# Kernel optimization log

Measured on AMD Instinct MI355X. Metric: run time of the kernel, lower is better.

Reference implementation:

```python
import jax, jax.numpy as jnp
import numpy as np

D_MODEL, D_BLOOM, N_HEADS = 768, 64, 4
HEAD_DIM = D_MODEL // N_HEADS


def setup_inputs() -> dict:
    key = jax.random.key(0)
    ks = jax.random.split(key, 16)
    B, S = 8, 1024
    s = 0.02
    return {
        "dnabert_hidden": jax.random.normal(ks[0], (B, S, D_MODEL), jnp.float32),
        "bloom_encoding": jax.random.uniform(ks[1], (B, S, D_BLOOM), jnp.float32),
        "Wq": jax.random.normal(ks[2], (D_MODEL, D_MODEL), jnp.float32) * s,
        "bq": jnp.zeros((D_MODEL,), jnp.float32),
        "Wk": jax.random.normal(ks[3], (D_BLOOM, D_MODEL), jnp.float32) * s,
        "bk": jnp.zeros((D_MODEL,), jnp.float32),
        "Wv": jax.random.normal(ks[4], (D_MODEL, D_MODEL), jnp.float32) * s,
        "bv": jnp.zeros((D_MODEL,), jnp.float32),
        "Wb1": jax.random.normal(ks[5], (D_BLOOM, N_HEADS * 2), jnp.float32) * s,
        "bb1": jnp.zeros((N_HEADS * 2,), jnp.float32),
        "Wb2": jax.random.normal(ks[6], (N_HEADS * 2, N_HEADS), jnp.float32) * s,
        "bb2": jnp.zeros((N_HEADS,), jnp.float32),
        "Wo": jax.random.normal(ks[7], (D_MODEL, D_MODEL), jnp.float32) * s,
        "bo": jnp.zeros((D_MODEL,), jnp.float32),
        "ln_g": jnp.ones((D_MODEL,), jnp.float32),
        "ln_b": jnp.zeros((D_MODEL,), jnp.float32),
    }


def reference(dnabert_hidden, bloom_encoding, Wq, bq, Wk, bk, Wv, bv,
              Wb1, bb1, Wb2, bb2, Wo, bo, ln_g, ln_b):
    B, S, _ = dnabert_hidden.shape
    H, Dh = N_HEADS, HEAD_DIM
    # projections -> [B, H, S, Dh]
    Q = (dnabert_hidden @ Wq + bq).reshape(B, S, H, Dh).transpose(0, 2, 1, 3)
    K = (bloom_encoding @ Wk + bk).reshape(B, S, H, Dh).transpose(0, 2, 1, 3)
    V = (dnabert_hidden @ Wv + bv).reshape(B, S, H, Dh).transpose(0, 2, 1, 3)
    scores = jnp.einsum('bhqd,bhkd->bhqk', Q, K) / jnp.sqrt(jnp.float32(Dh))
    # bloom bias MLP: [B, S, H] -> broadcast over query positions as [B, H, 1, S]
    h = jax.nn.gelu(bloom_encoding @ Wb1 + bb1, approximate=False)
    bias = (h @ Wb2 + bb2).transpose(0, 2, 1)[:, :, None, :]
    attn = jax.nn.softmax(scores + bias, axis=-1)  # dropout is identity in eval
    ctx = jnp.einsum('bhqk,bhkd->bhqd', attn, V)
    ctx = ctx.transpose(0, 2, 1, 3).reshape(B, S, H * Dh)
    out = ctx @ Wo + bo
    x = out + dnabert_hidden
    mu = jnp.mean(x, axis=-1, keepdims=True)
    var = jnp.var(x, axis=-1, keepdims=True)
    y = (x - mu) * jax.lax.rsqrt(var + 1e-5) * ln_g + ln_b
    return y, attn
```

## Files before the change

### kernel.cpp

```cpp
#include <hip/hip_runtime.h>
#include <hip/hip_bf16.h>
#include <math.h>
#include <stdint.h>

typedef __bf16 bf16;
typedef __bf16 bf16x8 __attribute__((ext_vector_type(8)));
typedef __bf16 bf16x4v __attribute__((ext_vector_type(4)));
typedef float f32x4 __attribute__((ext_vector_type(4)));

#define NHEADS 4
#define DM 768
#define DB 64
#define HD 192
#define BATCH 8
#define SEQ 1024
#define MROWS 8192
#define SCALE 0.07216878364870323f

__device__ __forceinline__ void gld_lds16(const void* g, void* l) {
  __builtin_amdgcn_global_load_lds(
      (__attribute__((address_space(1))) void*)(void*)g,
      (__attribute__((address_space(3))) void*)l, 16, 0, 0);
}

__global__ __launch_bounds__(256) void prologue(
    const float* __restrict__ Xd, bf16* __restrict__ Xd_bf,
    const float* __restrict__ Xb, bf16* __restrict__ Xb_bf,
    const float* __restrict__ Wq, const float* __restrict__ Wv,
    const float* __restrict__ Wk, const float* __restrict__ Wo,
    bf16* __restrict__ WT0, bf16* __restrict__ WT1,
    bf16* __restrict__ WT2, bf16* __restrict__ WT3,
    const float* __restrict__ Wb1, const float* __restrict__ bb1,
    const float* __restrict__ Wb2, const float* __restrict__ bb2,
    float* __restrict__ biasarr) {
  __shared__ float Lt[64 * 65];
  const int id = blockIdx.x;
  const int tid = threadIdx.x;
  if (id < 6656) {
    const float* in = (id < 6144) ? Xd : Xb;
    bf16* out = (id < 6144) ? Xd_bf : Xb_bf;
    long i = (long)(id < 6144 ? id : id - 6144) * 256 + tid;
    f32x4 v = *(const f32x4*)&in[i * 4];
    bf16x4v t;
    t[0] = (bf16)v[0]; t[1] = (bf16)v[1]; t[2] = (bf16)v[2]; t[3] = (bf16)v[3];
    *(bf16x4v*)&out[i * 4] = t;
  } else if (id < 6688) {
    int idx = (id - 6656) * 256 + tid;
    const float* x = Xb + (long)idx * DB;
    float h[8];
#pragma unroll
    for (int j = 0; j < 8; ++j) h[j] = bb1[j];
    for (int k = 0; k < DB; ++k) {
      float xv = x[k];
#pragma unroll
      for (int j = 0; j < 8; ++j) h[j] = fmaf(xv, Wb1[k * 8 + j], h[j]);
    }
#pragma unroll
    for (int j = 0; j < 8; ++j) {
      float a = h[j];
      h[j] = 0.5f * a * (1.0f + erff(a * 0.7071067811865476f));
    }
    int b = idx >> 10, s = idx & 1023;
#pragma unroll
    for (int o = 0; o < 4; ++o) {
      float a = bb2[o];
#pragma unroll
      for (int j = 0; j < 8; ++j) a = fmaf(h[j], Wb2[j * 4 + o], a);
      biasarr[((long)(b * 4 + o) << 10) + s] = a;
    }
  } else {
    int wi = id - 6688;
    const float* W;
    bf16* WT;
    int K, tIdx;
    if (wi < 144)      { W = Wq; WT = WT0; K = DM; tIdx = wi; }
    else if (wi < 288) { W = Wv; WT = WT1; K = DM; tIdx = wi - 144; }
    else if (wi < 300) { W = Wk; WT = WT2; K = DB; tIdx = wi - 288; }
    else               { W = Wo; WT = WT3; K = DM; tIdx = wi - 300; }
    const int tk0 = (tIdx / 12) * 64;
    const int tn0 = (tIdx % 12) * 64;
#pragma unroll
    for (int p = 0; p < 4; ++p) {
      int r = p * 16 + (tid >> 4);
      int c = (tid & 15) * 4;
      f32x4 v = *(const f32x4*)&W[(long)(tk0 + r) * DM + tn0 + c];
      Lt[r * 65 + c] = v[0]; Lt[r * 65 + c + 1] = v[1];
      Lt[r * 65 + c + 2] = v[2]; Lt[r * 65 + c + 3] = v[3];
    }
    __syncthreads();
    const int n = tid >> 2, kg = (tid & 3) * 16;
    bf16x8 o0, o1;
#pragma unroll
    for (int e = 0; e < 8; ++e) {
      o0[e] = (bf16)Lt[(kg + e) * 65 + n];
      o1[e] = (bf16)Lt[(kg + 8 + e) * 65 + n];
    }
    *(bf16x8*)&WT[(long)(tn0 + n) * K + tk0 + kg] = o0;
    *(bf16x8*)&WT[(long)(tn0 + n) * K + tk0 + kg + 8] = o1;
  }
}

__global__ __launch_bounds__(256) void rowsum_scale_f32(float* __restrict__ attn) {
  const int row = blockIdx.x * 4 + (threadIdx.x >> 6);
  const int lane = threadIdx.x & 63;
  float* ar = attn + ((long)row << 10);
  f32x4 v[4];
#pragma unroll
  for (int i = 0; i < 4; ++i) v[i] = *(const f32x4*)&ar[i * 256 + lane * 4];
  float s = 0.0f;
#pragma unroll
  for (int i = 0; i < 4; ++i)
#pragma unroll
    for (int j = 0; j < 4; ++j) s += v[i][j];
  for (int d = 1; d < 64; d <<= 1) s += __shfl_xor(s, d);
  float iv = 1.0f / s;
#pragma unroll
  for (int i = 0; i < 4; ++i) {
#pragma unroll
    for (int j = 0; j < 4; ++j) v[i][j] *= iv;
    *(f32x4*)&ar[i * 256 + lane * 4] = v[i];
  }
}

__global__ __launch_bounds__(256) void pv_attn(
    const bf16* __restrict__ E, const bf16* __restrict__ VT,
    const float* __restrict__ part, bf16* __restrict__ ctx,
    float* __restrict__ attn) {
  __shared__ __attribute__((aligned(16))) bf16 aL[2 * 64 * 32];
  __shared__ __attribute__((aligned(16))) bf16 bL[2 * 192 * 32];
  __shared__ float ivL[64];
  const int tid = threadIdx.x;
  const int lane = tid & 63;
  const int wid = tid >> 6;
  const int wr = wid >> 1, wc = wid & 1;
  const int id = blockIdx.x;
  const int bz = id & 31;
  const int by = id >> 5;
  const int m0 = by * 64;
  const int b = bz >> 2, h = bz & 3;

  const bf16* Ab = E + ((long)bz << 20);
  const bf16* Bb = VT + (((long)(b * DM + h * HD)) << 10);

  if (tid < 64) {
    const float* p = part + ((((long)bz << 10) + m0 + tid) << 4);
    float s = 0.0f;
#pragma unroll
    for (int i = 0; i < 16; ++i) s += p[i];
    ivL[tid] = 1.0f / s;
  }
  __syncthreads();
  const float iv0 = ivL[tid >> 2];

  f32x4 acc[2][6] = {};
  const int rsel = lane & 15, ksel = (lane >> 4) * 8;

  for (int k0 = 0; k0 < SEQ; k0 += 64) {
#pragma unroll
    for (int h2 = 0; h2 < 2; ++h2) {
      {
        int f = tid * 8;
        int row = f >> 5, col = f & 31;
        gld_lds16(Ab + (long)(m0 + row) * SEQ + k0 + h2 * 32 + col, &aL[h2 * 2048 + f]);
      }
#pragma unroll
      for (int p = 0; p < 3; ++p) {
        int f = (p * 256 + tid) * 8;
        int row = f >> 5, col = f & 31;
        gld_lds16(Bb + (long)row * SEQ + k0 + h2 * 32 + col, &bL[h2 * 6144 + f]);
      }
    }
    __syncthreads();

#pragma unroll
    for (int h2 = 0; h2 < 2; ++h2) {
      int f = tid * 8;
      int row = f >> 5, col = f & 31;
      bf16x8 e = *(const bf16x8*)&aL[h2 * 2048 + f];
      f32x4 w0, w1;
      w0[0] = (float)e[0] * iv0; w0[1] = (float)e[1] * iv0;
      w0[2] = (float)e[2] * iv0; w0[3] = (float)e[3] * iv0;
      w1[0] = (float)e[4] * iv0; w1[1] = (float)e[5] * iv0;
      w1[2] = (float)e[6] * iv0; w1[3] = (float)e[7] * iv0;
      float* ap = attn + ((long)bz << 20) + ((long)(m0 + row) << 10) + k0 + h2 * 32 + col;
      __builtin_nontemporal_store(w0, (f32x4*)ap);
      __builtin_nontemporal_store(w1, (f32x4*)(ap + 4));
    }

#pragma unroll
    for (int h2 = 0; h2 < 2; ++h2) {
      bf16x8 af[2], bfr[6];
#pragma unroll
      for (int m = 0; m < 2; ++m)
        af[m] = *(const bf16x8*)&aL[h2 * 2048 + (wr * 32 + m * 16 + rsel) * 32 + ksel];
#pragma unroll
      for (int n = 0; n < 6; ++n)
        bfr[n] = *(const bf16x8*)&bL[h2 * 6144 + (wc * 96 + n * 16 + rsel) * 32 + ksel];
#pragma unroll
      for (int m = 0; m < 2; ++m)
#pragma unroll
        for (int n = 0; n < 6; ++n)
          acc[m][n] = __builtin_amdgcn_mfma_f32_16x16x32_bf16(af[m], bfr[n], acc[m][n], 0, 0, 0);
    }
    __syncthreads();
  }

  const int rl = (lane >> 4) * 4, cl = lane & 15;
#pragma unroll
  for (int m = 0; m < 2; ++m)
#pragma unroll
    for (int n = 0; n < 6; ++n)
#pragma unroll
      for (int j = 0; j < 4; ++j) {
        int row = wr * 32 + m * 16 + rl + j;
        int col = wc * 96 + n * 16 + cl;
        bL[row * 192 + col] = (bf16)(acc[m][n][j] * ivL[row]);
      }
  __syncthreads();
#pragma unroll
  for (int it = 0; it < 6; ++it) {
    int idx2 = it * 256 + tid;
    int row = idx2 / 24;
    int col = (idx2 % 24) * 8;
    bf16x8 v = *(const bf16x8*)&bL[row * 192 + col];
    *(bf16x8*)&ctx[(long)(b * SEQ + m0 + row) * DM + h * HD + col] = v;
  }
}

template <int MODE>
__global__ __launch_bounds__(256) void gemm_bt(
    const bf16* __restrict__ A, int lda,
    const bf16* __restrict__ BT, int ldb,
    const float* __restrict__ Af,
    int M, int N, int Kd,
    const float* __restrict__ cb1,
    const float* __restrict__ cb2,
    const float* __restrict__ resid,
    void* __restrict__ out, void* __restrict__ out2) {
  __shared__ __attribute__((aligned(16))) bf16 aL[2 * 128 * 32];
  __shared__ __attribute__((aligned(16))) bf16 bL[2 * 128 * 32];
  const int tid = threadIdx.x;
  const int lane = tid & 63;
  const int wid = tid >> 6;
  const int wr = wid >> 1, wc = wid & 1;
  int bx, by, bz;
  if constexpr (MODE == 2 || MODE == 7) {
    int idd = blockIdx.x;
    bz = idd & 31;
    int t = idd >> 5;
    bx = t & 7;
    by = t >> 3;
  } else if constexpr (MODE == 5) {
    int idd = blockIdx.x;
    bz = idd & 31;
    bx = (idd >> 5) & 1;
    by = idd >> 6;
  } else {
    int idd = blockIdx.x;
    by = idd & 63;
    bx = idd >> 6;
    bz = 0;
  }
  const int m0 = by * 128, n0 = bx * 128;

  const bf16* Ab = A;
  const bf16* Bb = BT;
  const float* Afb = Af;
  if constexpr (MODE == 2 || MODE == 7) {
    long o = ((long)((bz >> 2) * SEQ)) * DM + (long)(bz & 3) * HD;
    Ab = A + o;
    Bb = BT + o;
  }
  if constexpr (MODE == 5) {
    Bb = BT + (((long)((bz >> 2) * DM + (bz & 3) * HD)) << 10);
    Afb = Af + ((long)bz << 20);
  }

  f32x4 acc[4][4] = {};

  for (int k0 = 0; k0 < Kd; k0 += 64) {
#pragma unroll
    for (int h = 0; h < 2; ++h) {
      if constexpr (MODE == 5) {
#pragma unroll
        for (int p = 0; p < 2; ++p) {
          int f = (p * 256 + tid) * 8;
          int row = f >> 5, col = f & 31;
          const float* g = Afb + (long)(m0 + row) * lda + k0 + h * 32 + col;
          f32x4 x0 = *(const f32x4*)g;
          f32x4 x1 = *(const f32x4*)(g + 4);
          bf16x8 t;
          t[0] = (bf16)x0[0]; t[1] = (bf16)x0[1]; t[2] = (bf16)x0[2]; t[3] = (bf16)x0[3];
          t[4] = (bf16)x1[0]; t[5] = (bf16)x1[1]; t[6] = (bf16)x1[2]; t[7] = (bf16)x1[3];
          *(bf16x8*)&aL[h * 4096 + f] = t;
        }
      } else {
#pragma unroll
        for (int p = 0; p < 2; ++p) {
          int f = (p * 256 + tid) * 8;
          int row = f >> 5, col = f & 31;
          gld_lds16(Ab + (long)(m0 + row) * lda + k0 + h * 32 + col, &aL[h * 4096 + f]);
        }
      }
#pragma unroll
      for (int p = 0; p < 2; ++p) {
        int f = (p * 256 + tid) * 8;
        int row = f >> 5, col = f & 31;
        int nn = n0 + row;
        nn = nn < N ? nn : N - 1;
        gld_lds16(Bb + (long)nn * ldb + k0 + h * 32 + col, &bL[h * 4096 + f]);
      }
    }
    __syncthreads();

    const int rsel = lane & 15, ksel = (lane >> 4) * 8;
#pragma unroll
    for (int h = 0; h < 2; ++h) {
      bf16x8 af[4], bfr[4];
#pragma unroll
      for (int m = 0; m < 4; ++m)
        af[m] = *(const bf16x8*)&aL[h * 4096 + (wr * 64 + m * 16 + rsel) * 32 + ksel];
#pragma unroll
      for (int n = 0; n < 4; ++n)
        bfr[n] = *(const bf16x8*)&bL[h * 4096 + (wc * 64 + n * 16 + rsel) * 32 + ksel];
#pragma unroll
      for (int m = 0; m < 4; ++m)
#pragma unroll
        for (int n = 0; n < 4; ++n)
          acc[m][n] = __builtin_amdgcn_mfma_f32_16x16x32_bf16(af[m], bfr[n], acc[m][n], 0, 0, 0);
    }
    __syncthreads();
  }

  const int rl = (lane >> 4) * 4, cl = lane & 15;

  if constexpr (MODE == 2) {
    float bvv[4];
#pragma unroll
    for (int n = 0; n < 4; ++n)
      bvv[n] = cb2[(bz << 10) + n0 + wc * 64 + n * 16 + cl];
#pragma unroll
    for (int m = 0; m < 4; ++m)
#pragma unroll
      for (int n = 0; n < 4; ++n)
#pragma unroll
        for (int j = 0; j < 4; ++j)
          acc[m][n][j] = __expf(fmaf(acc[m][n][j], SCALE, bvv[n]));
    float* part = (float*)out2;
#pragma unroll
    for (int m = 0; m < 4; ++m) {
#pragma unroll
      for (int j = 0; j < 4; ++j) {
        float s = acc[m][0][j] + acc[m][1][j] + acc[m][2][j] + acc[m][3][j];
#pragma unroll
        for (int d = 1; d < 16; d <<= 1) s += __shfl_xor(s, d);
        if (cl == 0) {
          int mg = m0 + wr * 64 + m * 16 + rl + j;
          part[((((long)bz << 10) + mg) << 4) + bx * 2 + wc] = s;
        }
      }
    }
#pragma unroll
    for (int m = 0; m < 4; ++m)
#pragma unroll
      for (int n = 0; n < 4; ++n)
#pragma unroll
        for (int j = 0; j < 4; ++j) {
          int row = wr * 64 + m * 16 + rl + j;
          int col = wc * 64 + n * 16 + cl;
          bf16* Lt = (row < 64) ? &aL[row * 128 + col] : &bL[(row - 64) * 128 + col];
          *Lt = (bf16)acc[m][n][j];
        }
    __syncthreads();
#pragma unroll
    for (int it = 0; it < 8; ++it) {
      int row = it * 16 + (tid >> 4);
      int col = (tid & 15) * 8;
      bf16x8 v = (row < 64) ? *(const bf16x8*)&aL[row * 128 + col]
                            : *(const bf16x8*)&bL[(row - 64) * 128 + col];
      *(bf16x8*)&((bf16*)out)[((long)bz << 20) + ((long)(m0 + row) << 10) + n0 + col] = v;
    }
    return;
  }

  if constexpr (MODE == 6) {
    if (n0 >= DM) {
      const int d0 = n0 - DM;
      float bvv[4];
#pragma unroll
      for (int n = 0; n < 4; ++n)
        bvv[n] = cb2[d0 + wc * 64 + n * 16 + cl];
#pragma unroll
      for (int m = 0; m < 4; ++m)
#pragma unroll
        for (int n = 0; n < 4; ++n)
#pragma unroll
          for (int j = 0; j < 4; ++j) {
            int row = wr * 64 + m * 16 + rl + j;
            int col = wc * 64 + n * 16 + cl;
            int sw = row ^ ((col & 7) << 4);
            bf16 val = (bf16)(acc[m][n][j] + bvv[n]);
            if (col < 64) aL[col * 128 + sw] = val;
            else          bL[(col - 64) * 128 + sw] = val;
          }
      __syncthreads();
      const int b = m0 >> 10, s0 = m0 & 1023;
#pragma unroll
      for (int it = 0; it < 8; ++it) {
        int d = it * 16 + (tid >> 4);
        int s = (tid & 15) * 8;
        int sw = s ^ ((d & 7) << 4);
        bf16x8 v = (d < 64) ? *(const bf16x8*)&aL[d * 128 + sw]
                            : *(const bf16x8*)&bL[(d - 64) * 128 + sw];
        *(bf16x8*)&((bf16*)out2)[((long)(b * DM + d0 + d) << 10) + s0 + s] = v;
      }
      return;
    }
  }

  if constexpr (MODE == 0 || MODE == 6) {
    float bvv[4];
#pragma unroll
    for (int n = 0; n < 4; ++n)
      bvv[n] = cb1[n0 + wc * 64 + n * 16 + cl];
#pragma unroll
    for (int m = 0; m < 4; ++m)
#pragma unroll
      for (int n = 0; n < 4; ++n)
#pragma unroll
        for (int j = 0; j < 4; ++j) {
          int row = wr * 64 + m * 16 + rl + j;
          int col = wc * 64 + n * 16 + cl;
          bf16 val = (bf16)(acc[m][n][j] + bvv[n]);
          if (row < 64) aL[row * 128 + col] = val;
          else          bL[(row - 64) * 128 + col] = val;
        }
    __syncthreads();
#pragma unroll
    for (int it = 0; it < 8; ++it) {
      int row = it * 16 + (tid >> 4);
      int col = (tid & 15) * 8;
      bf16x8 v = (row < 64) ? *(const bf16x8*)&aL[row * 128 + col]
                            : *(const bf16x8*)&bL[(row - 64) * 128 + col];
      *(bf16x8*)&((bf16*)out)[(long)(m0 + row) * DM + n0 + col] = v;
    }
    return;
  }

#pragma unroll
  for (int m = 0; m < 4; ++m) {
#pragma unroll
    for (int n = 0; n < 4; ++n) {
      int ng = n0 + wc * 64 + n * 16 + cl;
      if (ng >= N) continue;
#pragma unroll
      for (int j = 0; j < 4; ++j) {
        int mg = m0 + wr * 64 + m * 16 + rl + j;
        float v = acc[m][n][j];
        if constexpr (MODE == 7) {
          ((float*)out)[((long)bz << 20) + ((long)mg << 10) + ng] =
              __expf(fmaf(v, SCALE, cb2[(bz << 10) + ng]));
        } else if constexpr (MODE == 5) {
          ((bf16*)out)[(long)((bz >> 2) * SEQ + mg) * DM + (bz & 3) * HD + ng] = (bf16)v;
        } else {
          long o = (long)mg * DM + ng;
          ((float*)out)[o] = v + cb1[ng] + resid[o];
        }
      }
    }
  }
}

__global__ __launch_bounds__(256) void layernorm_rows(float* x, const float* __restrict__ gam,
                                                      const float* __restrict__ bet) {
  int row = blockIdx.x * 4 + (threadIdx.x >> 6);
  int lane = threadIdx.x & 63;
  float* r = x + (long)row * DM;
  f32x4 v[3];
#pragma unroll
  for (int i = 0; i < 3; ++i) v[i] = *(const f32x4*)&r[i * 256 + lane * 4];
  float s = 0.0f, ss = 0.0f;
#pragma unroll
  for (int i = 0; i < 3; ++i)
#pragma unroll
    for (int j = 0; j < 4; ++j) {
      s += v[i][j];
      ss += v[i][j] * v[i][j];
    }
  for (int d = 1; d < 64; d <<= 1) {
    s += __shfl_xor(s, d);
    ss += __shfl_xor(ss, d);
  }
  float mu = s * (1.0f / 768.0f);
  float var = ss * (1.0f / 768.0f) - mu * mu;
  float rs = 1.0f / sqrtf(var + 1e-5f);
#pragma unroll
  for (int i = 0; i < 3; ++i) {
#pragma unroll
    for (int j = 0; j < 4; ++j) {
      int c = i * 256 + lane * 4 + j;
      v[i][j] = (v[i][j] - mu) * rs * gam[c] + bet[c];
    }
    *(f32x4*)&r[i * 256 + lane * 4] = v[i];
  }
}

extern "C" void kernel_launch(void* const* d_in, const int* in_sizes, int n_in,
                              void* d_out, int out_size, void* d_ws, size_t ws_size,
                              hipStream_t stream) {
  const float* Xd = (const float*)d_in[0];
  const float* Xb = (const float*)d_in[1];
  const float* Wq = (const float*)d_in[2];
  const float* bq = (const float*)d_in[3];
  const float* Wk = (const float*)d_in[4];
  const float* bk = (const float*)d_in[5];
  const float* Wv = (const float*)d_in[6];
  const float* bv = (const float*)d_in[7];
  const float* Wb1 = (const float*)d_in[8];
  const float* bb1 = (const float*)d_in[9];
  const float* Wb2 = (const float*)d_in[10];
  const float* bb2 = (const float*)d_in[11];
  const float* Wo = (const float*)d_in[12];
  const float* bo = (const float*)d_in[13];
  const float* lng = (const float*)d_in[14];
  const float* lnb = (const float*)d_in[15];

  float* y = (float*)d_out;
  float* attn = y + (long)MROWS * DM;

  char* w = (char*)d_ws;
  bf16* Xd_bf = (bf16*)w; w += (long)MROWS * DM * 2;
  bf16* Xb_bf = (bf16*)w; w += (long)MROWS * DB * 2;
  bf16* WqvT = (bf16*)w; w += (long)2 * DM * DM * 2;
  bf16* WkT = (bf16*)w; w += (long)DM * DB * 2;
  bf16* WoT = (bf16*)w; w += (long)DM * DM * 2;
  bf16* Qb = (bf16*)w; w += (long)MROWS * DM * 2;
  bf16* Kb = (bf16*)w; w += (long)MROWS * DM * 2;
  bf16* VTb = (bf16*)w; w += (long)MROWS * DM * 2;
  float* biasarr = (float*)w; w += (long)BATCH * NHEADS * SEQ * 4;
  float* part = (float*)w; w += (long)32 * SEQ * 16 * 4;
  bf16* Sb = (bf16*)w; w += (long)32 * SEQ * SEQ * 2;
  const bool useS = ((size_t)(w - (char*)d_ws)) <= ws_size;
  bf16* ctxb = Xd_bf;

  dim3 blk(256);
  prologue<<<7132, blk, 0, stream>>>(Xd, Xd_bf, Xb, Xb_bf, Wq, Wv, Wk, Wo,
                                     WqvT, WqvT + (long)DM * DM, WkT, WoT,
                                     Wb1, bb1, Wb2, bb2, biasarr);

  gemm_bt<0><<<384, blk, 0, stream>>>(Xb_bf, DB, WkT, DB, nullptr, MROWS, DM, DB,
                                      bk, nullptr, nullptr, Kb, nullptr);
  gemm_bt<6><<<768, blk, 0, stream>>>(Xd_bf, DM, WqvT, DM, nullptr, MROWS, 2 * DM, DM,
                                      bq, bv, nullptr, Qb, VTb);
  if (useS) {
    gemm_bt<2><<<2048, blk, 0, stream>>>(Qb, DM, Kb, DM, nullptr, SEQ, SEQ, HD,
                                         nullptr, biasarr, nullptr, Sb, part);
    pv_attn<<<512, blk, 0, stream>>>(Sb, VTb, part, ctxb, attn);
  } else {
    gemm_bt<7><<<2048, blk, 0, stream>>>(Qb, DM, Kb, DM, nullptr, SEQ, SEQ, HD,
                                         nullptr, biasarr, nullptr, attn, nullptr);
    rowsum_scale_f32<<<8192, blk, 0, stream>>>(attn);
    gemm_bt<5><<<512, blk, 0, stream>>>(nullptr, SEQ, VTb, SEQ, attn, SEQ, HD, SEQ,
                                        nullptr, nullptr, nullptr, ctxb, nullptr);
  }
  gemm_bt<4><<<384, blk, 0, stream>>>(ctxb, DM, WoT, DM, nullptr, MROWS, DM, DM,
                                      bo, nullptr, Xd, y, nullptr);
  layernorm_rows<<<2048, 256, 0, stream>>>(y, lng, lnb);
}
```

Baseline: 175.7 us.

## Merge K and QV projection GEMMs into one launch; stage Wo epilogue via LDS

Replaces the two projection GEMM launches (K from the bloom encoding, Q/V from the hidden states) with a single kernel whose blocks branch by block index. This saves one launch and lets the small K blocks fill the tail of the larger Q/V work. The Wo GEMM epilogue now stages fp32 accumulators through shared memory in two halves, so the bias-plus-residual add and the output store become coalesced 16-byte accesses instead of scalar strided writes. The risks are extra barriers and shared-memory traffic in the epilogue. The merged kernel also uses a simple single-stage load loop that may differ from the original gemm_bt pipelining.

```diff
diff --git a/kernel.cpp b/kernel.cpp
--- a/kernel.cpp
+++ b/kernel.cpp
@@ -97,6 +97,137 @@
     }
     *(bf16x8*)&WT[(long)(tn0 + n) * K + tk0 + kg] = o0;
     *(bf16x8*)&WT[(long)(tn0 + n) * K + tk0 + kg + 8] = o1;
+  }
+}
+
+__global__ __launch_bounds__(256) void proj_all(
+    const bf16* __restrict__ Xb_bf, const bf16* __restrict__ WkT,
+    const bf16* __restrict__ Xd_bf, const bf16* __restrict__ WqvT,
+    const float* __restrict__ bk, const float* __restrict__ bq,
+    const float* __restrict__ bv,
+    bf16* __restrict__ Kb, bf16* __restrict__ Qb, bf16* __restrict__ VTb) {
+  __shared__ __attribute__((aligned(16))) bf16 aL[2 * 128 * 32];
+  __shared__ __attribute__((aligned(16))) bf16 bL[2 * 128 * 32];
+  const int tid = threadIdx.x;
+  const int lane = tid & 63;
+  const int wid = tid >> 6;
+  const int wr = wid >> 1, wc = wid & 1;
+  const int id = blockIdx.x;
+  const bool isK = id < 384;
+  int by, bx, lda, Kd, N;
+  const bf16 *A, *BT;
+  if (isK) {
+    by = id & 63; bx = id >> 6;
+    A = Xb_bf; BT = WkT; lda = DB; Kd = DB; N = DM;
+  } else {
+    int t = id - 384;
+    by = t & 63; bx = t >> 6;
+    A = Xd_bf; BT = WqvT; lda = DM; Kd = DM; N = 2 * DM;
+  }
+  const int m0 = by * 128, n0 = bx * 128;
+
+  f32x4 acc[4][4] = {};
+
+  for (int k0 = 0; k0 < Kd; k0 += 64) {
+#pragma unroll
+    for (int h = 0; h < 2; ++h) {
+#pragma unroll
+      for (int p = 0; p < 2; ++p) {
+        int f = (p * 256 + tid) * 8;
+        int row = f >> 5, col = f & 31;
+        gld_lds16(A + (long)(m0 + row) * lda + k0 + h * 32 + col, &aL[h * 4096 + f]);
+      }
+#pragma unroll
+      for (int p = 0; p < 2; ++p) {
+        int f = (p * 256 + tid) * 8;
+        int row = f >> 5, col = f & 31;
+        int nn = n0 + row;
+        nn = nn < N ? nn : N - 1;
+        gld_lds16(BT + (long)nn * lda + k0 + h * 32 + col, &bL[h * 4096 + f]);
+      }
+    }
+    __syncthreads();
+
+    const int rsel = lane & 15, ksel = (lane >> 4) * 8;
+#pragma unroll
+    for (int h = 0; h < 2; ++h) {
+      bf16x8 af[4], bfr[4];
+#pragma unroll
+      for (int m = 0; m < 4; ++m)
+        af[m] = *(const bf16x8*)&aL[h * 4096 + (wr * 64 + m * 16 + rsel) * 32 + ksel];
+#pragma unroll
+      for (int n = 0; n < 4; ++n)
+        bfr[n] = *(const bf16x8*)&bL[h * 4096 + (wc * 64 + n * 16 + rsel) * 32 + ksel];
+#pragma unroll
+      for (int m = 0; m < 4; ++m)
+#pragma unroll
+        for (int n = 0; n < 4; ++n)
+          acc[m][n] = __builtin_amdgcn_mfma_f32_16x16x32_bf16(af[m], bfr[n], acc[m][n], 0, 0, 0);
+    }
+    __syncthreads();
+  }
+
+  const int rl = (lane >> 4) * 4, cl = lane & 15;
+
+  if (!isK && n0 >= DM) {
+    const int d0 = n0 - DM;
+    float bvv[4];
+#pragma unroll
+    for (int n = 0; n < 4; ++n)
+      bvv[n] = bv[d0 + wc * 64 + n * 16 + cl];
+#pragma unroll
+    for (int m = 0; m < 4; ++m)
+#pragma unroll
+      for (int n = 0; n < 4; ++n)
+#pragma unroll
+        for (int j = 0; j < 4; ++j) {
+          int row = wr * 64 + m * 16 + rl + j;
+          int col = wc * 64 + n * 16 + cl;
+          int sw = row ^ ((col & 7) << 4);
+          bf16 val = (bf16)(acc[m][n][j] + bvv[n]);
+          if (col < 64) aL[col * 128 + sw] = val;
+          else          bL[(col - 64) * 128 + sw] = val;
+        }
+    __syncthreads();
+    const int b = m0 >> 10, s0 = m0 & 1023;
+#pragma unroll
+    for (int it = 0; it < 8; ++it) {
+      int d = it * 16 + (tid >> 4);
+      int s = (tid & 15) * 8;
+      int sw = s ^ ((d & 7) << 4);
+      bf16x8 v = (d < 64) ? *(const bf16x8*)&aL[d * 128 + sw]
+                          : *(const bf16x8*)&bL[(d - 64) * 128 + sw];
+      *(bf16x8*)&VTb[((long)(b * DM + d0 + d) << 10) + s0 + s] = v;
+    }
+    return;
+  }
+
+  const float* cb = isK ? bk : bq;
+  bf16* out = isK ? Kb : Qb;
+  float bvv[4];
+#pragma unroll
+  for (int n = 0; n < 4; ++n)
+    bvv[n] = cb[n0 + wc * 64 + n * 16 + cl];
+#pragma unroll
+  for (int m = 0; m < 4; ++m)
+#pragma unroll
+    for (int n = 0; n < 4; ++n)
+#pragma unroll
+      for (int j = 0; j < 4; ++j) {
+        int row = wr * 64 + m * 16 + rl + j;
+        int col = wc * 64 + n * 16 + cl;
+        bf16 val = (bf16)(acc[m][n][j] + bvv[n]);
+        if (row < 64) aL[row * 128 + col] = val;
+        else          bL[(row - 64) * 128 + col] = val;
+      }
+  __syncthreads();
+#pragma unroll
+  for (int it = 0; it < 8; ++it) {
+    int row = it * 16 + (tid >> 4);
+    int col = (tid & 15) * 8;
+    bf16x8 v = (row < 64) ? *(const bf16x8*)&aL[row * 128 + col]
+                          : *(const bf16x8*)&bL[(row - 64) * 128 + col];
+    *(bf16x8*)&out[(long)(m0 + row) * DM + n0 + col] = v;
   }
 }
 
@@ -383,66 +514,41 @@
     return;
   }
 
-  if constexpr (MODE == 6) {
-    if (n0 >= DM) {
-      const int d0 = n0 - DM;
-      float bvv[4];
-#pragma unroll
-      for (int n = 0; n < 4; ++n)
-        bvv[n] = cb2[d0 + wc * 64 + n * 16 + cl];
-#pragma unroll
-      for (int m = 0; m < 4; ++m)
-#pragma unroll
-        for (int n = 0; n < 4; ++n)
-#pragma unroll
-          for (int j = 0; j < 4; ++j) {
-            int row = wr * 64 + m * 16 + rl + j;
-            int col = wc * 64 + n * 16 + cl;
-            int sw = row ^ ((col & 7) << 4);
-            bf16 val = (bf16)(acc[m][n][j] + bvv[n]);
-            if (col < 64) aL[col * 128 + sw] = val;
-            else          bL[(col - 64) * 128 + sw] = val;
-          }
+  if constexpr (MODE == 4) {
+#pragma unroll
+    for (int half = 0; half < 2; ++half) {
+      if (wr == half) {
+#pragma unroll
+        for (int m = 0; m < 4; ++m)
+#pragma unroll
+          for (int n = 0; n < 4; ++n)
+#pragma unroll
+            for (int j = 0; j < 4; ++j) {
+              int r = m * 16 + rl + j;
+              int col = wc * 64 + n * 16 + cl;
+              float* Lf = (r < 32) ? (float*)aL + r * 128
+                                   : (float*)bL + (r - 32) * 128;
+              Lf[col] = acc[m][n][j];
+            }
+      }
       __syncthreads();
-      const int b = m0 >> 10, s0 = m0 & 1023;
 #pragma unroll
       for (int it = 0; it < 8; ++it) {
-        int d = it * 16 + (tid >> 4);
-        int s = (tid & 15) * 8;
-        int sw = s ^ ((d & 7) << 4);
-        bf16x8 v = (d < 64) ? *(const bf16x8*)&aL[d * 128 + sw]
-                            : *(const bf16x8*)&bL[(d - 64) * 128 + sw];
-        *(bf16x8*)&((bf16*)out2)[((long)(b * DM + d0 + d) << 10) + s0 + s] = v;
-      }
-      return;
-    }
-  }
-
-  if constexpr (MODE == 0 || MODE == 6) {
-    float bvv[4];
-#pragma unroll
-    for (int n = 0; n < 4; ++n)
-      bvv[n] = cb1[n0 + wc * 64 + n * 16 + cl];
-#pragma unroll
-    for (int m = 0; m < 4; ++m)
-#pragma unroll
-      for (int n = 0; n < 4; ++n)
-#pragma unroll
-        for (int j = 0; j < 4; ++j) {
-          int row = wr * 64 + m * 16 + rl + j;
-          int col = wc * 64 + n * 16 + cl;
-          bf16 val = (bf16)(acc[m][n][j] + bvv[n]);
-          if (row < 64) aL[row * 128 + col] = val;
-          else          bL[(row - 64) * 128 + col] = val;
-        }
-    __syncthreads();
-#pragma unroll
-    for (int it = 0; it < 8; ++it) {
-      int row = it * 16 + (tid >> 4);
-      int col = (tid & 15) * 8;
-      bf16x8 v = (row < 64) ? *(const bf16x8*)&aL[row * 128 + col]
-                            : *(const bf16x8*)&bL[(row - 64) * 128 + col];
-      *(bf16x8*)&((bf16*)out)[(long)(m0 + row) * DM + n0 + col] = v;
+        int r = it * 8 + (tid >> 5);
+        int c = (tid & 31) * 4;
+        const float* Lf = (r < 32) ? (const float*)aL + r * 128
+                                   : (const float*)bL + (r - 32) * 128;
+        f32x4 v = *(const f32x4*)&Lf[c];
+        long o = (long)(m0 + half * 64 + r) * DM + n0 + c;
+        f32x4 rs = *(const f32x4*)&resid[o];
+        f32x4 y;
+        y[0] = v[0] + cb1[n0 + c] + rs[0];
+        y[1] = v[1] + cb1[n0 + c + 1] + rs[1];
+        y[2] = v[2] + cb1[n0 + c + 2] + rs[2];
+        y[3] = v[3] + cb1[n0 + c + 3] + rs[3];
+        *(f32x4*)&((float*)out)[o] = y;
+      }
+      __syncthreads();
     }
     return;
   }
@@ -462,9 +568,6 @@
               __expf(fmaf(v, SCALE, cb2[(bz << 10) + ng]));
         } else if constexpr (MODE == 5) {
           ((bf16*)out)[(long)((bz >> 2) * SEQ + mg) * DM + (bz & 3) * HD + ng] = (bf16)v;
-        } else {
-          long o = (long)mg * DM + ng;
-          ((float*)out)[o] = v + cb1[ng] + resid[o];
         }
       }
     }
@@ -548,10 +651,8 @@
                                      WqvT, WqvT + (long)DM * DM, WkT, WoT,
                                      Wb1, bb1, Wb2, bb2, biasarr);
 
-  gemm_bt<0><<<384, blk, 0, stream>>>(Xb_bf, DB, WkT, DB, nullptr, MROWS, DM, DB,
-                                      bk, nullptr, nullptr, Kb, nullptr);
-  gemm_bt<6><<<768, blk, 0, stream>>>(Xd_bf, DM, WqvT, DM, nullptr, MROWS, 2 * DM, DM,
-                                      bq, bv, nullptr, Qb, VTb);
+  proj_all<<<1152, blk, 0, stream>>>(Xb_bf, WkT, Xd_bf, WqvT, bk, bq, bv, Kb, Qb, VTb);
+
   if (useS) {
     gemm_bt<2><<<2048, blk, 0, stream>>>(Qb, DM, Kb, DM, nullptr, SEQ, SEQ, HD,
                                          nullptr, biasarr, nullptr, Sb, part);
```

Result: no change. 172.6 us (-1.8%).
